# Performance work log

Hardware: AMD Instinct MI355X
Metric: run time of the kernel (lower is better)

Reference implementation:

```python
import jax, jax.numpy as jnp
import numpy as np
from jax import lax

B, C, H, W = 2, 64, 48, 48
NH, DK, DV = 8, 64, 128          # heads, per-head d_k, per-head d_v
DN, NS, R = 128, 16, 4           # SS2D d_inner (expand=2), d_state, dt_rank
MULT = 4                          # FFN expansion
L = H * W


def layer_norm(x, w, b, eps=1e-5):
    m = x.mean(-1, keepdims=True)
    v = ((x - m) ** 2).mean(-1, keepdims=True)
    return (x - m) / jnp.sqrt(v + eps) * w + b


def conv2d(x, w, groups=1):
    # x: NCHW, w: OIHW
    return lax.conv_general_dilated(x, w, (1, 1), 'SAME',
                                    dimension_numbers=('NCHW', 'OIHW', 'NCHW'),
                                    feature_group_count=groups)


def setup_inputs() -> dict:
    key = jax.random.key(0)
    ks = jax.random.split(key, 24)
    rn = lambda k, shp, s=0.02: jax.random.normal(k, shp, jnp.float32) * s
    inp = {
        'enc_input': jax.random.normal(ks[0], (B, C, H, W), jnp.float32),
        'slf_attn_snr': jax.random.uniform(ks[1], (B, 1, H, W), jnp.float32),
        # MultiHeadAttention params
        'attn_wq': rn(ks[2], (C, NH * DK)),
        'attn_wk': rn(ks[3], (C, NH * DK)),
        'attn_wv': rn(ks[4], (C, NH * DV)),
        'attn_fc': rn(ks[5], (NH * DV, C)),
        'attn_ln_w': jnp.ones((C,), jnp.float32),
        'attn_ln_b': jnp.zeros((C,), jnp.float32),
        # SS2D params
        'ss_in_w': rn(ks[6], (C, 2 * DN)),
        'ss_conv_w': rn(ks[7], (DN, 1, 3, 3)),
        'ss_conv_b': jnp.zeros((DN,), jnp.float32),
        'ss_xproj_w': rn(ks[8], (4, R + 2 * NS, DN)),
        'ss_dt_w': rn(ks[9], (4, DN, R)),
        'ss_dt_b': rn(ks[10], (4, DN)),
        'ss_Alog': jnp.log(jnp.broadcast_to(jnp.arange(1, NS + 1, dtype=jnp.float32), (4, DN, NS))),
        'ss_D': jnp.ones((4, DN), jnp.float32),
        'ss_norm_w': jnp.ones((DN,), jnp.float32),
        'ss_norm_b': jnp.zeros((DN,), jnp.float32),
        'ss_out_w': rn(ks[11], (DN, C)),
        # FFN (PreNorm + conv block)
        'ffn_ln_w': jnp.ones((C,), jnp.float32),
        'ffn_ln_b': jnp.zeros((C,), jnp.float32),
        'ffn_w1': rn(ks[12], (C * MULT, C, 1, 1)),
        'ffn_dw': rn(ks[13], (C * MULT, 1, 3, 3)),
        'ffn_w2': rn(ks[14], (C, C * MULT, 1, 1)),
    }
    return inp


def reference(enc_input, slf_attn_snr, attn_wq, attn_wk, attn_wv, attn_fc,
              attn_ln_w, attn_ln_b, ss_in_w, ss_conv_w, ss_conv_b, ss_xproj_w,
              ss_dt_w, ss_dt_b, ss_Alog, ss_D, ss_norm_w, ss_norm_b, ss_out_w,
              ffn_ln_w, ffn_ln_b, ffn_w1, ffn_dw, ffn_w2):
    # ---- Multi-head self-attention over spatial tokens (SNR-biased) ----
    x_tok = enc_input.reshape(B, C, L).transpose(0, 2, 1)        # (B, L, C)
    q = (x_tok @ attn_wq).reshape(B, L, NH, DK).transpose(0, 2, 1, 3)
    k = (x_tok @ attn_wk).reshape(B, L, NH, DK).transpose(0, 2, 1, 3)
    v = (x_tok @ attn_wv).reshape(B, L, NH, DV).transpose(0, 2, 1, 3)
    scores = jnp.einsum('bhqd,bhkd->bhqk', q, k) / jnp.sqrt(jnp.float32(DK))
    snr_flat = slf_attn_snr.reshape(B, 1, 1, L)                  # bias over keys
    scores = scores + jnp.log(snr_flat + 1e-4)
    attn = jax.nn.softmax(scores, axis=-1)                       # (B, NH, L, L)
    o = jnp.einsum('bhqk,bhkd->bhqd', attn, v)
    o = o.transpose(0, 2, 1, 3).reshape(B, L, NH * DV) @ attn_fc
    enc_output = layer_norm(o + x_tok, attn_ln_w, attn_ln_b)     # post-LN residual
    enc_output = enc_output.transpose(0, 2, 1).reshape(B, C, H, W)

    # ---- SS2D: 4-direction 2D selective scan ----
    xh = enc_output.transpose(0, 2, 3, 1)                        # (B, H, W, C)
    snr_h = slf_attn_snr.transpose(0, 2, 3, 1)                   # (B, H, W, 1)
    xz = xh @ ss_in_w                                            # (B, H, W, 2*DN)
    x1, z = xz[..., :DN], xz[..., DN:]
    x1 = x1.transpose(0, 3, 1, 2)                                # (B, DN, H, W)
    x1 = conv2d(x1, ss_conv_w, groups=DN) + ss_conv_b[None, :, None, None]
    x1 = jax.nn.silu(x1)

    x_hw = x1.reshape(B, DN, L)
    x_wh = x1.transpose(0, 1, 3, 2).reshape(B, DN, L)
    xs = jnp.stack([x_hw, x_wh], axis=1)                         # (B, 2, DN, L)
    xs = jnp.concatenate([xs, jnp.flip(xs, axis=-1)], axis=1)    # (B, 4, DN, L)

    x_dbl = jnp.einsum('bkdl,kcd->bkcl', xs, ss_xproj_w)
    dts, Bs, Cs = x_dbl[:, :, :R], x_dbl[:, :, R:R + NS], x_dbl[:, :, R + NS:]
    dts = jnp.einsum('bkrl,kdr->bkdl', dts, ss_dt_w) + ss_dt_b[None, :, :, None]
    dts = jax.nn.softplus(dts)                                   # (B, 4, DN, L)
    A = -jnp.exp(ss_Alog)                                        # (4, DN, NS)

    def step(h, inp):
        xt, dtt, Bt, Ct = inp                                    # (B,4,DN),(B,4,DN),(B,4,NS),(B,4,NS)
        dA = jnp.exp(dtt[..., None] * A)                         # (B,4,DN,NS)
        h = h * dA + (dtt * xt)[..., None] * Bt[:, :, None, :]
        y = jnp.einsum('bkdn,bkn->bkd', h, Ct)
        return h, y

    h0 = jnp.zeros((B, 4, DN, NS), jnp.float32)
    elems = (xs.transpose(3, 0, 1, 2), dts.transpose(3, 0, 1, 2),
             Bs.transpose(3, 0, 1, 2), Cs.transpose(3, 0, 1, 2))
    _, ys = lax.scan(step, h0, elems)                            # (L, B, 4, DN)
    ys = ys.transpose(1, 2, 3, 0) + ss_D[None, :, :, None] * xs  # (B, 4, DN, L)

    inv = jnp.flip(ys[:, 2:4], axis=-1)                          # undo reversed scans
    wh = ys[:, 1].reshape(B, DN, W, H).transpose(0, 1, 3, 2).reshape(B, DN, L)
    invwh = inv[:, 1].reshape(B, DN, W, H).transpose(0, 1, 3, 2).reshape(B, DN, L)
    y = ys[:, 0] + inv[:, 0] + wh + invwh                        # (B, DN, L)
    y = y.transpose(0, 2, 1).reshape(B, H, W, DN)
    y = layer_norm(y, ss_norm_w, ss_norm_b) * jax.nn.silu(z) * snr_h
    x2 = y @ ss_out_w + enc_input.transpose(0, 2, 3, 1)          # (B, H, W, C)

    # ---- PreNorm conv FeedForward ----
    xn = layer_norm(x2, ffn_ln_w, ffn_ln_b).transpose(0, 3, 1, 2)
    h1 = jax.nn.gelu(conv2d(xn, ffn_w1), approximate=False)
    h1 = jax.nn.gelu(conv2d(h1, ffn_dw, groups=C * MULT), approximate=False)
    h1 = conv2d(h1, ffn_w2).transpose(0, 2, 3, 1)
    x3 = h1 + x2

    return x3.transpose(0, 3, 1, 2)                              # (B, C, H, W)
```

## Files before the change

### kernel.cpp

```cpp
#include <hip/hip_runtime.h>
#include <hip/hip_bf16.h>

#define Bq 2
#define Cc 64
#define Hh 48
#define Ww 48
#define Ll 2304
#define NHh 8
#define DKk 64
#define DVv 128
#define DNn 128
#define NSs 16
#define Rr 4
#define SCH 48
#define SNC 48
#define TT 8
#define TT2 16

#define OQ    0u
#define OK_   2359296u
#define OV    4718592u
#define OO    9437184u
#define OX1P  14450688u
#define OZ    15040512u
#define OVT   15630336u
#define OLP   (OVT + 2359296u)
#define OFCB  (OVT + 2433024u)
#define OX2   0u
#define WS_NEED_FLOATS (OVT + 4718592u)
#define ODT2  OQ
#define OYS2  OK_
#define OX1S  (OV + 1179648u)
#define OBS2  (OV + 1769472u)
#define OCS2  (OV + 2064384u)
#define OCSA  (OV + 2359296u)
#define OCSB  (OV + 3145728u)
#define OHST  (OV + 3932160u)
#define OH1A  OO
#define OH1B  (OO + 1179648u)

typedef short short8v __attribute__((ext_vector_type(8)));
typedef short short4v __attribute__((ext_vector_type(4)));
typedef float f32x4 __attribute__((ext_vector_type(4)));
typedef unsigned short ushort_t;

__device__ __forceinline__ float geluf(float x) {
  return 0.5f * x * (1.0f + erff(x * 0.70710678118654752f));
}
__device__ __forceinline__ float siluf(float x) {
  return x / (1.0f + __expf(-x));
}
__device__ __forceinline__ float softplusf(float x) {
  return fmaxf(x, 0.0f) + log1pf(__expf(-fabsf(x)));
}
__device__ __forceinline__ int spmap(int k, int l) {
  if (k == 0) return l;
  if (k == 1) return (l % 48) * 48 + l / 48;
  if (k == 2) return 2303 - l;
  int l2 = 2303 - l; return (l2 % 48) * 48 + l2 / 48;
}
__device__ __forceinline__ short f2bf(float f) {
  unsigned u = __float_as_uint(f);
  unsigned r = (u + 0x7FFFu + ((u >> 16) & 1u)) >> 16;
  return (short)r;
}
__device__ __forceinline__ float bfu2f(ushort_t u) {
  return __uint_as_float(((unsigned)u) << 16);
}

__global__ void k_code(float* out) { if (threadIdx.x == 0) out[0] = 25000.f; }

__global__ __launch_bounds__(256) void k_qkv(const float* __restrict__ enc,
    const float* __restrict__ wq, const float* __restrict__ wk,
    const float* __restrict__ wv, float* __restrict__ ws) {
  int l0 = blockIdx.x * TT; int b = blockIdx.y;
  int t = threadIdx.x;
  __shared__ float xs[64][12];
  {
    int idx = t, c = idx >> 3, i = idx & 7;
    xs[c][i] = enc[(size_t)b * Cc * Ll + (size_t)c * Ll + l0 + i];
    idx = t + 256; c = idx >> 3; i = idx & 7;
    xs[c][i] = enc[(size_t)b * Cc * Ll + (size_t)c * Ll + l0 + i];
  }
  __syncthreads();
  ushort_t* qb = (ushort_t*)(ws + OQ);
  ushort_t* kb = (ushort_t*)(ws + OK_);
  float* v = ws + OV;
#pragma unroll
  for (int g = 0; g < 6; ++g) {
    int j = t + g * 256;
    float acc[TT];
#pragma unroll
    for (int i = 0; i < TT; ++i) acc[i] = 0.f;
    const float* wp; int col, stride;
    if (j < 512) { wp = wq + j; stride = 512; col = j; }
    else if (j < 1024) { wp = wk + (j - 512); stride = 512; col = j - 512; }
    else { wp = wv + (j - 1024); stride = 1024; col = j - 1024; }
    for (int c = 0; c < 64; ++c) {
      float w = wp[(size_t)c * stride];
      const float4* xc = (const float4*)&xs[c][0];
      float4 x0 = xc[0], x1 = xc[1];
      acc[0] += x0.x * w; acc[1] += x0.y * w;
      acc[2] += x0.z * w; acc[3] += x0.w * w;
      acc[4] += x1.x * w; acc[5] += x1.y * w;
      acc[6] += x1.z * w; acc[7] += x1.w * w;
    }
    if (j < 512) {
#pragma unroll
      for (int i = 0; i < TT; ++i)
        qb[((size_t)(b * 8 + (col >> 6)) * Ll + l0 + i) * 64 + (col & 63)] =
            (ushort_t)f2bf(acc[i] * 0.125f);
    } else if (j < 1024) {
#pragma unroll
      for (int i = 0; i < TT; ++i)
        kb[((size_t)(b * 8 + (col >> 6)) * Ll + l0 + i) * 64 + (col & 63)] =
            (ushort_t)f2bf(acc[i]);
    } else {
#pragma unroll
      for (int i = 0; i < TT; ++i)
        v[((size_t)(b * 8 + (col >> 7)) * Ll + l0 + i) * 128 + (col & 127)] = acc[i];
    }
  }
}

__global__ __launch_bounds__(256) void k_vt(float* __restrict__ ws) {
  int bh = blockIdx.y;
  int l0 = blockIdx.x * 64;
  int t = threadIdx.x;
  __shared__ float tile[128][65];
  const float* vp = ws + OV + ((size_t)bh * Ll + l0) * 128;
  for (int i = t; i < 64 * 32; i += 256) {
    int l = i >> 5, dv4 = (i & 31) * 4;
    float4 a = *(const float4*)(vp + (size_t)l * 128 + dv4);
    tile[dv4][l] = a.x; tile[dv4 + 1][l] = a.y;
    tile[dv4 + 2][l] = a.z; tile[dv4 + 3][l] = a.w;
  }
  __syncthreads();
  ushort_t* vt = (ushort_t*)(ws + OVT) + (size_t)bh * 128 * Ll + l0;
  for (int i = t; i < 128 * 16; i += 256) {
    int dv = i >> 4, l4 = (i & 15) * 4;
    short4v a;
    a[0] = f2bf(tile[dv][l4]); a[1] = f2bf(tile[dv][l4 + 1]);
    a[2] = f2bf(tile[dv][l4 + 2]); a[3] = f2bf(tile[dv][l4 + 3]);
    *(short4v*)(vt + (size_t)dv * Ll + l4) = a;
  }
}

__global__ __launch_bounds__(256) void k_fcbf(const float* __restrict__ fc,
                                              float* __restrict__ ws) {
  int col = blockIdx.x;
  int t = threadIdx.x;
  ushort_t* dst = (ushort_t*)(ws + OFCB) + (size_t)col * 1024;
  for (int k = t; k < 1024; k += 256)
    dst[k] = (ushort_t)f2bf(fc[(size_t)k * 64 + col]);
}

#define NKT2 18
#define LSK 72
__global__ __launch_bounds__(256) void k_attn(const float* __restrict__ snr,
                                              float* __restrict__ ws) {
  int bh = blockIdx.y; int b = bh >> 3; int hd = bh & 7;
  int q0 = blockIdx.x * 64;
  int ks = blockIdx.z;
  int kbase = ks * (Ll / 2);
  int t = threadIdx.x;
  int w = t >> 6, lane = t & 63;
  int m16 = lane & 15, quad = lane >> 4;

  __shared__ __align__(16) ushort_t Ks[64 * LSK];
  __shared__ __align__(16) ushort_t Vs[128 * LSK];
  __shared__ __align__(16) ushort_t Ps[4 * 16 * LSK];
  __shared__ float sfac_s[64];

  const ushort_t* qbf = (const ushort_t*)(ws + OQ) + (size_t)bh * Ll * 64;
  const ushort_t* kbf = (const ushort_t*)(ws + OK_) + (size_t)bh * Ll * 64;
  const ushort_t* vtb = (const ushort_t*)(ws + OVT) + (size_t)bh * 128 * Ll;

  short8v qa[2];
  {
    const ushort_t* qrp = qbf + (size_t)(q0 + w * 16 + m16) * 64 + quad * 8;
    qa[0] = *(const short8v*)qrp;
    qa[1] = *(const short8v*)(qrp + 32);
  }
  int sk_key = t >> 2, sk_d0 = (t & 3) * 16;
  int sv_dv = t >> 1, sv_k0 = (t & 1) * 32;

  short8v kreg[2], vreg[4];
  float snr_reg = 0.f;
  {
    const ushort_t* ksrc = kbf + (size_t)(kbase + sk_key) * 64 + sk_d0;
    kreg[0] = *(const short8v*)ksrc;
    kreg[1] = *(const short8v*)(ksrc + 8);
    const ushort_t* vsrc = vtb + (size_t)sv_dv * Ll + kbase + sv_k0;
#pragma unroll
    for (int i = 0; i < 4; ++i) vreg[i] = *(const short8v*)(vsrc + i * 8);
    if (t < 64) snr_reg = snr[b * Ll + kbase + t];
  }

  f32x4 oacc[8];
#pragma unroll
  for (int i = 0; i < 8; ++i) oacc[i] = (f32x4)0.f;
  float l_r[4] = {0.f, 0.f, 0.f, 0.f};

  for (int kt = 0; kt < NKT2; ++kt) {
    __syncthreads();
    *(short8v*)&Ks[sk_key * LSK + sk_d0] = kreg[0];
    *(short8v*)&Ks[sk_key * LSK + sk_d0 + 8] = kreg[1];
#pragma unroll
    for (int i = 0; i < 4; ++i)
      *(short8v*)&Vs[sv_dv * LSK + sv_k0 + i * 8] = vreg[i];
    if (t < 64) sfac_s[t] = snr_reg + 1e-4f;
    __syncthreads();
    if (kt + 1 < NKT2) {
      int k0n = kbase + (kt + 1) * 64;
      const ushort_t* ksrc = kbf + (size_t)(k0n + sk_key) * 64 + sk_d0;
      kreg[0] = *(const short8v*)ksrc;
      kreg[1] = *(const short8v*)(ksrc + 8);
      const ushort_t* vsrc = vtb + (size_t)sv_dv * Ll + k0n + sv_k0;
#pragma unroll
      for (int i = 0; i < 4; ++i) vreg[i] = *(const short8v*)(vsrc + i * 8);
      if (t < 64) snr_reg = snr[b * Ll + k0n + t];
    }

    f32x4 sac[4];
#pragma unroll
    for (int n = 0; n < 4; ++n) {
      int key = n * 16 + m16;
      short8v kb0 = *(const short8v*)&Ks[key * LSK + quad * 8];
      short8v kb1 = *(const short8v*)&Ks[key * LSK + 32 + quad * 8];
      f32x4 acc = (f32x4)0.f;
      acc = __builtin_amdgcn_mfma_f32_16x16x32_bf16(qa[0], kb0, acc, 0, 0, 0);
      acc = __builtin_amdgcn_mfma_f32_16x16x32_bf16(qa[1], kb1, acc, 0, 0, 0);
      sac[n] = acc;
    }
    float sf[4];
#pragma unroll
    for (int n = 0; n < 4; ++n) sf[n] = sfac_s[n * 16 + m16];
    ushort_t* pw = &Ps[w * 16 * LSK];
#pragma unroll
    for (int r = 0; r < 4; ++r) {
#pragma unroll
      for (int n = 0; n < 4; ++n) {
        float p = __expf(sac[n][r]) * sf[n];
        l_r[r] += p;
        pw[(quad * 4 + r) * LSK + n * 16 + m16] = (ushort_t)f2bf(p);
      }
    }
    short8v pb0 = *(const short8v*)&pw[m16 * LSK + quad * 8];
    short8v pb1 = *(const short8v*)&pw[m16 * LSK + 32 + quad * 8];
#pragma unroll
    for (int dt_ = 0; dt_ < 8; ++dt_) {
      const ushort_t* vrow = &Vs[(dt_ * 16 + m16) * LSK];
      short8v va0 = *(const short8v*)&vrow[quad * 8];
      short8v va1 = *(const short8v*)&vrow[32 + quad * 8];
      f32x4 o = oacc[dt_];
      o = __builtin_amdgcn_mfma_f32_16x16x32_bf16(va0, pb0, o, 0, 0, 0);
      o = __builtin_amdgcn_mfma_f32_16x16x32_bf16(va1, pb1, o, 0, 0, 0);
      oacc[dt_] = o;
    }
  }
#pragma unroll
  for (int r = 0; r < 4; ++r) {
    float lv = l_r[r];
    lv += __shfl_xor(lv, 1, 64);
    lv += __shfl_xor(lv, 2, 64);
    lv += __shfl_xor(lv, 4, 64);
    lv += __shfl_xor(lv, 8, 64);
    l_r[r] = lv;
  }
  if (m16 == 0) {
    float* lp = ws + OLP + (size_t)ks * (Bq * NHh * Ll) + (size_t)bh * Ll;
#pragma unroll
    for (int r = 0; r < 4; ++r) lp[q0 + w * 16 + quad * 4 + r] = l_r[r];
  }
  ushort_t* opb = (ushort_t*)(ws + (ks ? OV : OO));
  ushort_t* op = opb + ((size_t)(b * Ll + q0 + w * 16 + m16)) * 1024 + hd * 128;
#pragma unroll
  for (int dt_ = 0; dt_ < 8; ++dt_) {
    short4v o4;
#pragma unroll
    for (int r = 0; r < 4; ++r) o4[r] = f2bf(oacc[dt_][r]);
    *(short4v*)&op[dt_ * 16 + quad * 4] = o4;
  }
}

__global__ __launch_bounds__(256) void k_oprojxz(const float* __restrict__ enc,
    const float* __restrict__ lnw, const float* __restrict__ lnb,
    const float* __restrict__ ssin, float* __restrict__ ws) {
  int l0 = blockIdx.x * TT2, b = blockIdx.y, t = threadIdx.x;
  int w = t >> 6, lane = t & 63, m16 = lane & 15, quad = lane >> 4;
  __shared__ __align__(16) ushort_t obf[16][1040];
  __shared__ float linv_s[8][16];
  __shared__ float part[16][68];
  __shared__ float xh_s[64][17];
  if (t < 128) {
    int hd = t >> 4, i = t & 15;
    float l1 = ws[OLP + (size_t)(b * 8 + hd) * Ll + l0 + i];
    float l2 = ws[OLP + (size_t)(Bq * NHh * Ll) + (size_t)(b * 8 + hd) * Ll + l0 + i];
    linv_s[hd][i] = 1.f / (l1 + l2);
  }
  __syncthreads();
  const ushort_t* p0 = (const ushort_t*)(ws + OO) + (size_t)(b * Ll + l0) * 1024;
  const ushort_t* p1 = (const ushort_t*)(ws + OV) + (size_t)(b * Ll + l0) * 1024;
#pragma unroll
  for (int g = 0; g < 8; ++g) {
    int v = t + g * 256;
    int tok = v >> 7, k0 = (v & 127) * 8;
    short8v a = *(const short8v*)(p0 + (size_t)tok * 1024 + k0);
    short8v bb = *(const short8v*)(p1 + (size_t)tok * 1024 + k0);
    float li = linv_s[k0 >> 7][tok];
    short8v o;
#pragma unroll
    for (int j = 0; j < 8; ++j)
      o[j] = f2bf((bfu2f((ushort_t)a[j]) + bfu2f((ushort_t)bb[j])) * li);
    *(short8v*)&obf[tok][k0] = o;
  }
  __syncthreads();
  f32x4 cacc = (f32x4)0.f;
  const ushort_t* fcb = (const ushort_t*)(ws + OFCB) +
                        (size_t)(w * 16 + m16) * 1024 + quad * 8;
#pragma unroll
  for (int kb = 0; kb < 32; ++kb) {
    short8v a = *(const short8v*)&obf[m16][kb * 32 + quad * 8];
    short8v bf = *(const short8v*)(fcb + kb * 32);
    cacc = __builtin_amdgcn_mfma_f32_16x16x32_bf16(a, bf, cacc, 0, 0, 0);
  }
#pragma unroll
  for (int r = 0; r < 4; ++r) part[quad * 4 + r][w * 16 + m16] = cacc[r];
  __syncthreads();
  {
    int col = lane;
    float lw = lnw[col], lb = lnb[col];
#pragma unroll
    for (int i2 = 0; i2 < 4; ++i2) {
      int i = w * 4 + i2;
      float a = part[i][col] + enc[(size_t)b * Cc * Ll + (size_t)col * Ll + l0 + i];
      float s = a;
#pragma unroll
      for (int o = 32; o >= 1; o >>= 1) s += __shfl_xor(s, o, 64);
      float m = s * (1.f / 64.f);
      float dd = a - m;
      float vs = dd * dd;
#pragma unroll
      for (int o = 32; o >= 1; o >>= 1) vs += __shfl_xor(vs, o, 64);
      xh_s[col][i] = dd * rsqrtf(vs * (1.f / 64.f) + 1e-5f) * lw + lb;
    }
  }
  __syncthreads();
  {
    float acc2[TT2];
#pragma unroll
    for (int i = 0; i < TT2; ++i) acc2[i] = 0.f;
    for (int c = 0; c < 64; ++c) {
      float wv_ = ssin[c * 256 + t];
      const float* xc = &xh_s[c][0];
#pragma unroll
      for (int i = 0; i < TT2; ++i) acc2[i] += xc[i] * wv_;
    }
    if (t < 128) {
#pragma unroll
      for (int i = 0; i < TT2; ++i)
        ws[OX1P + ((size_t)(b * Ll + l0 + i)) * 128 + t] = acc2[i];
    } else {
#pragma unroll
      for (int i = 0; i < TT2; ++i)
        ws[OZ + ((size_t)(b * Ll + l0 + i)) * 128 + (t - 128)] = acc2[i];
    }
  }
}

__global__ __launch_bounds__(256) void k_conv(const float* __restrict__ cw,
    const float* __restrict__ cb, float* __restrict__ ws) {
  int l0 = blockIdx.x * TT, b = blockIdx.y, t = threadIdx.x;
  int h = l0 / 48, w0 = l0 % 48;
  __shared__ float tile[3][10][128];
  for (int idx = t; idx < 3840; idx += 256) {
    int r = idx / 1280, rem = idx % 1280;
    int col = rem >> 7, d = rem & 127;
    int hh = h + r - 1, wx = w0 + col - 1;
    float v = 0.f;
    if (hh >= 0 && hh < 48 && wx >= 0 && wx < 48)
      v = ws[OX1P + ((size_t)(b * Ll + hh * 48 + wx)) * 128 + d];
    tile[r][col][d] = v;
  }
  __syncthreads();
  int d = t & 127, half = t >> 7;
  float cwr[9];
#pragma unroll
  for (int j = 0; j < 9; ++j) cwr[j] = cw[d * 9 + j];
  float cbv = cb[d];
#pragma unroll
  for (int j = 0; j < 4; ++j) {
    int i = half * 4 + j;
    float acc = cbv;
#pragma unroll
    for (int kh = 0; kh < 3; ++kh)
#pragma unroll
      for (int kw = 0; kw < 3; ++kw)
        acc += tile[kh][i + kw][d] * cwr[kh * 3 + kw];
    ws[OX1S + ((size_t)(b * Ll + l0 + i)) * 128 + d] = siluf(acc);
  }
}

__global__ __launch_bounds__(128) void k_xdbl(const float* __restrict__ xw,
    const float* __restrict__ dtw, const float* __restrict__ dtb,
    float* __restrict__ ws) {
  int l0 = blockIdx.x * TT;
  int by = blockIdx.y; int b = by >> 2; int k = by & 3;
  int t = threadIdx.x;
  __shared__ float xv[128][9];
  __shared__ float pr[36][TT];
#pragma unroll
  for (int i = 0; i < TT; ++i) {
    int sp = spmap(k, l0 + i);
    xv[t][i] = ws[OX1S + ((size_t)(b * Ll) + sp) * 128 + t];
  }
  __syncthreads();
  if (t < 36) {
    float s[TT];
#pragma unroll
    for (int i = 0; i < TT; ++i) s[i] = 0.f;
    const float* wp = xw + (size_t)(k * 36 + t) * 128;
    for (int d = 0; d < 128; ++d) {
      float w = wp[d];
      const float* xc = &xv[d][0];
#pragma unroll
      for (int i = 0; i < TT; ++i) s[i] += xc[i] * w;
    }
#pragma unroll
    for (int i = 0; i < TT; ++i) pr[t][i] = s[i];
  }
  __syncthreads();
  {
    int d = t;
    const float* wp = dtw + (size_t)(k * 128 + d) * 4;
    float w0 = wp[0], w1 = wp[1], w2 = wp[2], w3 = wp[3];
    float bb = dtb[k * 128 + d];
#pragma unroll
    for (int i = 0; i < TT; ++i) {
      float v = pr[0][i] * w0 + pr[1][i] * w1 + pr[2][i] * w2 + pr[3][i] * w3 + bb;
      ws[ODT2 + ((size_t)(by * Ll + l0 + i)) * 128 + d] = softplusf(v);
    }
  }
  if (t < 16) {
#pragma unroll
    for (int i = 0; i < TT; ++i)
      ws[OBS2 + ((size_t)(by * Ll + l0 + i)) * 16 + t] = pr[4 + t][i];
  } else if (t < 32) {
#pragma unroll
    for (int i = 0; i < TT; ++i)
      ws[OCS2 + ((size_t)(by * Ll + l0 + i)) * 16 + (t - 16)] = pr[20 + (t - 16)][i];
  }
}

__global__ __launch_bounds__(256) void k_scanA(const float* __restrict__ alog,
                                               float* __restrict__ ws) {
  int c = blockIdx.x;
  int bk = blockIdx.y;
  int b = bk >> 2, k = bk & 3;
  int t = threadIdx.x;
  int n = t & 15, dg = t >> 4;
  __shared__ float dt_s[2][128], x_s[2][128], Bs_s[2][16];
  float A_r[8], ap[8], bc[8];
#pragma unroll
  for (int i = 0; i < 8; ++i) {
    int d = dg * 8 + i;
    A_r[i] = -__expf(alog[(size_t)((k * 128 + d) * 16) + n]);
    ap[i] = 1.f; bc[i] = 0.f;
  }
  const float* dtp = ws + ODT2 + ((size_t)bk * Ll) * 128;
  const float* bsp = ws + OBS2 + ((size_t)bk * Ll) * 16;
  const float* xb = ws + OX1S + (size_t)b * Ll * 128;
  float r_a = 0.f, r_Bs = 0.f;
  {
    int l = c * SCH;
    int sp = spmap(k, l);
    if (t < 128) r_a = dtp[(size_t)l * 128 + t];
    else r_a = xb[(size_t)sp * 128 + (t - 128)];
    if (t < 16) r_Bs = bsp[(size_t)l * 16 + t];
  }
  for (int ll = 0; ll < SCH; ++ll) {
    int buf = ll & 1;
    if (t < 128) dt_s[buf][t] = r_a;
    else x_s[buf][t - 128] = r_a;
    if (t < 16) Bs_s[buf][t] = r_Bs;
    __syncthreads();
    if (ll + 1 < SCH) {
      int l2 = c * SCH + ll + 1;
      int sp2 = spmap(k, l2);
      if (t < 128) r_a = dtp[(size_t)l2 * 128 + t];
      else r_a = xb[(size_t)sp2 * 128 + (t - 128)];
      if (t < 16) r_Bs = bsp[(size_t)l2 * 16 + t];
    }
    float Bv = Bs_s[buf][n];
#pragma unroll
    for (int i = 0; i < 8; ++i) {
      int d = dg * 8 + i;
      float dtv = dt_s[buf][d];
      float a = __expf(dtv * A_r[i]);
      bc[i] = bc[i] * a + dtv * x_s[buf][d] * Bv;
      ap[i] *= a;
    }
  }
  float* csa = ws + OCSA + ((size_t)(bk * SNC + c) * 128) * 16;
  float* csb = ws + OCSB + ((size_t)(bk * SNC + c) * 128) * 16;
#pragma unroll
  for (int i = 0; i < 8; ++i) {
    int d = dg * 8 + i;
    csa[d * 16 + n] = ap[i];
    csb[d * 16 + n] = bc[i];
  }
}

__global__ __launch_bounds__(256) void k_scanB(float* __restrict__ ws) {
  int g = blockIdx.x * 256 + threadIdx.x;
  int bk = g >> 11;
  int dn = g & 2047;
  const float* csa = ws + OCSA;
  const float* csb = ws + OCSB;
  float* hst = ws + OHST;
  size_t base = (size_t)bk * SNC * 2048 + dn;
  float h = 0.f;
  float a = csa[base], bq = csb[base];
  for (int c = 0; c < SNC; ++c) {
    float na = 0.f, nb = 0.f;
    if (c + 1 < SNC) {
      size_t idx2 = base + (size_t)(c + 1) * 2048;
      na = csa[idx2]; nb = csb[idx2];
    }
    hst[base + (size_t)c * 2048] = h;
    h = a * h + bq;
    a = na; bq = nb;
  }
}

__global__ __launch_bounds__(256) void k_scanC(const float* __restrict__ alog,
    const float* __restrict__ Dp, float* __restrict__ ws) {
  int c = blockIdx.x, bk = blockIdx.y;
  int b = bk >> 2, k = bk & 3;
  int t = threadIdx.x;
  int n = t & 15, dg = t >> 4;
  __shared__ float dt_s[2][128], x_s[2][128], Bs_s[2][16], Cs_s[2][16];
  float A_r[8], h[8], Dv[8];
#pragma unroll
  for (int i = 0; i < 8; ++i) {
    int d = dg * 8 + i;
    A_r[i] = -__expf(alog[(size_t)((k * 128 + d) * 16) + n]);
    h[i] = ws[OHST + ((size_t)(bk * SNC + c) * 128 + d) * 16 + n];
    Dv[i] = Dp[k * 128 + d];
  }
  const float* dtp = ws + ODT2 + ((size_t)bk * Ll) * 128;
  const float* bsp = ws + OBS2 + ((size_t)bk * Ll) * 16;
  const float* csp = ws + OCS2 + ((size_t)bk * Ll) * 16;
  const float* xb = ws + OX1S + (size_t)b * Ll * 128;
  float* yp = ws + OYS2 + ((size_t)bk * Ll) * 128;
  float r_a = 0.f, r_bc = 0.f;
  {
    int l = c * SCH;
    int sp = spmap(k, l);
    if (t < 128) r_a = dtp[(size_t)l * 128 + t];
    else r_a = xb[(size_t)sp * 128 + (t - 128)];
    if (t < 16) r_bc = bsp[(size_t)l * 16 + t];
    else if (t < 32) r_bc = csp[(size_t)l * 16 + (t - 16)];
  }
  for (int ll = 0; ll < SCH; ++ll) {
    int buf = ll & 1;
    if (t < 128) dt_s[buf][t] = r_a;
    else x_s[buf][t - 128] = r_a;
    if (t < 16) Bs_s[buf][t] = r_bc;
    else if (t < 32) Cs_s[buf][t - 16] = r_bc;
    __syncthreads();
    if (ll + 1 < SCH) {
      int l2 = c * SCH + ll + 1;
      int sp2 = spmap(k, l2);
      if (t < 128) r_a = dtp[(size_t)l2 * 128 + t];
      else r_a = xb[(size_t)sp2 * 128 + (t - 128)];
      if (t < 16) r_bc = bsp[(size_t)l2 * 16 + t];
      else if (t < 32) r_bc = csp[(size_t)l2 * 16 + (t - 16)];
    }
    int l = c * SCH + ll;
    float Bv = Bs_s[buf][n], Cv = Cs_s[buf][n];
    float yacc[8];
#pragma unroll
    for (int i = 0; i < 8; ++i) {
      int d = dg * 8 + i;
      float dtv = dt_s[buf][d];
      float a = __expf(dtv * A_r[i]);
      h[i] = h[i] * a + dtv * x_s[buf][d] * Bv;
      yacc[i] = h[i] * Cv;
    }
#pragma unroll
    for (int i = 0; i < 8; ++i) {
      float yv = yacc[i];
      yv += __shfl_xor(yv, 1, 64);
      yv += __shfl_xor(yv, 2, 64);
      yv += __shfl_xor(yv, 4, 64);
      yv += __shfl_xor(yv, 8, 64);
      yacc[i] = yv;
    }
    if (n == 0) {
#pragma unroll
      for (int i = 0; i < 8; ++i) {
        int d = dg * 8 + i;
        yp[(size_t)l * 128 + d] = yacc[i] + Dv[i] * x_s[buf][d];
      }
    }
  }
}

__global__ __launch_bounds__(256) void k_combffn1(const float* __restrict__ enc,
    const float* __restrict__ nw, const float* __restrict__ nb,
    const float* __restrict__ snr, const float* __restrict__ ow,
    const float* __restrict__ lw, const float* __restrict__ lb,
    const float* __restrict__ w1, float* __restrict__ ws) {
  int l0 = blockIdx.x * TT, b = blockIdx.y, t = threadIdx.x;
  __shared__ float yr[128][9];
  __shared__ float redm[2][TT], redq[2][TT];
  __shared__ float part[2][TT][64];
  __shared__ float xn_s[64][9];
  int lane = t & 63, wid = (t >> 6) & 1;
  float v[TT], m[TT];
  if (t < 128) {
    int d = t;
    const float* ysb = ws + OYS2;
#pragma unroll
    for (int i = 0; i < TT; ++i) {
      int l = l0 + i;
      int hh = l / 48, wwp = l % 48;
      int lT = wwp * 48 + hh;
      v[i] = ysb[((size_t)(b * 4 + 0) * Ll + l) * 128 + d] +
             ysb[((size_t)(b * 4 + 2) * Ll + (2303 - l)) * 128 + d] +
             ysb[((size_t)(b * 4 + 1) * Ll + lT) * 128 + d] +
             ysb[((size_t)(b * 4 + 3) * Ll + (2303 - lT)) * 128 + d];
    }
    float s[TT];
#pragma unroll
    for (int i = 0; i < TT; ++i) s[i] = v[i];
#pragma unroll
    for (int o = 32; o >= 1; o >>= 1)
#pragma unroll
      for (int i = 0; i < TT; ++i) s[i] += __shfl_xor(s[i], o, 64);
    if (lane == 0) {
#pragma unroll
      for (int i = 0; i < TT; ++i) redm[wid][i] = s[i];
    }
  }
  __syncthreads();
  if (t < 128) {
    float q[TT];
#pragma unroll
    for (int i = 0; i < TT; ++i) {
      m[i] = (redm[0][i] + redm[1][i]) * (1.f / 128.f);
      float dv = v[i] - m[i];
      q[i] = dv * dv;
    }
#pragma unroll
    for (int o = 32; o >= 1; o >>= 1)
#pragma unroll
      for (int i = 0; i < TT; ++i) q[i] += __shfl_xor(q[i], o, 64);
    if (lane == 0) {
#pragma unroll
      for (int i = 0; i < TT; ++i) redq[wid][i] = q[i];
    }
  }
  __syncthreads();
  if (t < 128) {
    int d = t;
    float nwv = nw[d], nbv = nb[d];
#pragma unroll
    for (int i = 0; i < TT; ++i) {
      int l = l0 + i;
      float var = (redq[0][i] + redq[1][i]) * (1.f / 128.f);
      float y = (v[i] - m[i]) * rsqrtf(var + 1e-5f) * nwv + nbv;
      float zv = ws[OZ + ((size_t)(b * Ll + l)) * 128 + d];
      y *= siluf(zv);
      y *= snr[b * Ll + l];
      yr[d][i] = y;
    }
  }
  __syncthreads();
  if (t < 128) {
    int col = t & 63, seg = t >> 6;
    float acc[TT];
#pragma unroll
    for (int i = 0; i < TT; ++i) acc[i] = 0.f;
    const float* ows = ow + (size_t)(seg * 64) * 64 + col;
    for (int c = 0; c < 64; ++c) {
      float w = ows[c * 64];
      const float* yc = &yr[seg * 64 + c][0];
#pragma unroll
      for (int i = 0; i < TT; ++i) acc[i] += yc[i] * w;
    }
#pragma unroll
    for (int i = 0; i < TT; ++i) part[seg][i][col] = acc[i];
  }
  __syncthreads();
  {
    int wv = t >> 6, col2 = t & 63;
    float lwv = lw[col2], lbv = lb[col2];
#pragma unroll
    for (int i2 = 0; i2 < 2; ++i2) {
      int i = wv * 2 + i2;
      float a = part[0][i][col2] + part[1][i][col2];
      a += enc[(size_t)b * Cc * Ll + (size_t)col2 * Ll + l0 + i];
      ws[OX2 + ((size_t)(b * Ll + l0 + i)) * 64 + col2] = a;
      float s = a;
#pragma unroll
      for (int o = 32; o >= 1; o >>= 1) s += __shfl_xor(s, o, 64);
      float mm = s * (1.f / 64.f);
      float dd2 = a - mm;
      float vs = dd2 * dd2;
#pragma unroll
      for (int o = 32; o >= 1; o >>= 1) vs += __shfl_xor(vs, o, 64);
      xn_s[col2][i] = dd2 * rsqrtf(vs * (1.f / 64.f) + 1e-5f) * lwv + lbv;
    }
  }
  __syncthreads();
  {
    float acc2[TT];
#pragma unroll
    for (int i = 0; i < TT; ++i) acc2[i] = 0.f;
    const float* wp = w1 + (size_t)t * 64;
    for (int c = 0; c < 64; ++c) {
      float w = wp[c];
      const float* xc = &xn_s[c][0];
#pragma unroll
      for (int i = 0; i < TT; ++i) acc2[i] += xc[i] * w;
    }
#pragma unroll
    for (int i = 0; i < TT; ++i)
      ws[OH1A + ((size_t)(b * Ll + l0 + i)) * 256 + t] = geluf(acc2[i]);
  }
}

__global__ __launch_bounds__(256) void k_ffndw(const float* __restrict__ dww,
                                               float* __restrict__ ws) {
  int l0 = blockIdx.x * TT, b = blockIdx.y, t = threadIdx.x;
  int h = l0 / 48, w0 = l0 % 48;
  __shared__ float tile[3][10][256];
  for (int idx = t; idx < 7680; idx += 256) {
    int r = idx / 2560, rem = idx % 2560;
    int col = rem >> 8, ch = rem & 255;
    int hh = h + r - 1, wx = w0 + col - 1;
    float v = 0.f;
    if (hh >= 0 && hh < 48 && wx >= 0 && wx < 48)
      v = ws[OH1A + ((size_t)(b * Ll + hh * 48 + wx)) * 256 + ch];
    tile[r][col][ch] = v;
  }
  __syncthreads();
  float dwr[9];
#pragma unroll
  for (int j = 0; j < 9; ++j) dwr[j] = dww[t * 9 + j];
#pragma unroll
  for (int i = 0; i < TT; ++i) {
    float acc = 0.f;
#pragma unroll
    for (int kh = 0; kh < 3; ++kh)
#pragma unroll
      for (int kw = 0; kw < 3; ++kw)
        acc += tile[kh][i + kw][t] * dwr[kh * 3 + kw];
    ws[OH1B + ((size_t)(b * Ll + l0 + i)) * 256 + t] = geluf(acc);
  }
}

__global__ __launch_bounds__(256) void k_ffn2(const float* __restrict__ w2,
                                              float* __restrict__ ws,
                                              float* __restrict__ out) {
  int l0 = blockIdx.x * TT, b = blockIdx.y, t = threadIdx.x;
  __shared__ float hr[256][9];
  __shared__ float part[4][TT][64];
  const float* hp = ws + OH1B + ((size_t)(b * Ll + l0)) * 256;
#pragma unroll
  for (int i = 0; i < TT; ++i) hr[t][i] = hp[(size_t)i * 256 + t];
  __syncthreads();
  int col = t & 63, seg = t >> 6;
  {
    float acc[TT];
#pragma unroll
    for (int i = 0; i < TT; ++i) acc[i] = 0.f;
    const float* wp = w2 + (size_t)col * 256 + seg * 64;
    for (int c = 0; c < 64; ++c) {
      float w = wp[c];
      const float* hc = &hr[seg * 64 + c][0];
#pragma unroll
      for (int i = 0; i < TT; ++i) acc[i] += hc[i] * w;
    }
#pragma unroll
    for (int i = 0; i < TT; ++i) part[seg][i][col] = acc[i];
  }
  __syncthreads();
  if (t < 64) {
    float av[TT];
#pragma unroll
    for (int i = 0; i < TT; ++i) {
      float a = part[0][i][t] + part[1][i][t] + part[2][i][t] + part[3][i][t];
      av[i] = a + ws[OX2 + ((size_t)(b * Ll + l0 + i)) * 64 + t];
    }
    float* opx = out + ((size_t)(b * 64 + t)) * 2304 + l0;
    *(float4*)opx = make_float4(av[0], av[1], av[2], av[3]);
    *((float4*)opx + 1) = make_float4(av[4], av[5], av[6], av[7]);
  }
}

extern "C" void kernel_launch(void* const* d_in, const int* in_sizes, int n_in,
                              void* d_out, int out_size, void* d_ws, size_t ws_size,
                              hipStream_t stream) {
  (void)in_sizes; (void)n_in; (void)out_size;
  const float* enc  = (const float*)d_in[0];
  const float* snr  = (const float*)d_in[1];
  const float* wq   = (const float*)d_in[2];
  const float* wk   = (const float*)d_in[3];
  const float* wv   = (const float*)d_in[4];
  const float* fc   = (const float*)d_in[5];
  const float* alnw = (const float*)d_in[6];
  const float* alnb = (const float*)d_in[7];
  const float* ssin = (const float*)d_in[8];
  const float* cw   = (const float*)d_in[9];
  const float* cb   = (const float*)d_in[10];
  const float* xw   = (const float*)d_in[11];
  const float* dtw  = (const float*)d_in[12];
  const float* dtb  = (const float*)d_in[13];
  const float* alog = (const float*)d_in[14];
  const float* Dp   = (const float*)d_in[15];
  const float* nw   = (const float*)d_in[16];
  const float* nb   = (const float*)d_in[17];
  const float* ow   = (const float*)d_in[18];
  const float* flnw = (const float*)d_in[19];
  const float* flnb = (const float*)d_in[20];
  const float* w1   = (const float*)d_in[21];
  const float* dww  = (const float*)d_in[22];
  const float* w2   = (const float*)d_in[23];
  float* ws = (float*)d_ws;
  float* out = (float*)d_out;

  if (ws_size < (size_t)WS_NEED_FLOATS * 4) {
    hipLaunchKernelGGL(k_code, dim3(1), dim3(64), 0, stream, out);
    return;
  }

  hipLaunchKernelGGL(k_qkv, dim3(Ll / TT, Bq), dim3(256), 0, stream, enc, wq, wk, wv, ws);
  hipLaunchKernelGGL(k_vt, dim3(Ll / 64, Bq * NHh), dim3(256), 0, stream, ws);
  hipLaunchKernelGGL(k_fcbf, dim3(64), dim3(256), 0, stream, fc, ws);
  hipLaunchKernelGGL(k_attn, dim3(Ll / 64, Bq * NHh, 2), dim3(256), 0, stream, snr, ws);
  hipLaunchKernelGGL(k_oprojxz, dim3(Ll / TT2, Bq), dim3(256), 0, stream, enc, alnw, alnb, ssin, ws);
  hipLaunchKernelGGL(k_conv, dim3(Ll / TT, Bq), dim3(256), 0, stream, cw, cb, ws);
  hipLaunchKernelGGL(k_xdbl, dim3(Ll / TT, Bq * 4), dim3(128), 0, stream, xw, dtw, dtb, ws);
  hipLaunchKernelGGL(k_scanA, dim3(SNC, Bq * 4), dim3(256), 0, stream, alog, ws);
  hipLaunchKernelGGL(k_scanB, dim3(64), dim3(256), 0, stream, ws);
  hipLaunchKernelGGL(k_scanC, dim3(SNC, Bq * 4), dim3(256), 0, stream, alog, Dp, ws);
  hipLaunchKernelGGL(k_combffn1, dim3(Ll / TT, Bq), dim3(256), 0, stream, enc, nw, nb, snr, ow, flnw, flnb, w1, ws);
  hipLaunchKernelGGL(k_ffndw, dim3(Ll / TT, Bq), dim3(256), 0, stream, dww, ws);
  hipLaunchKernelGGL(k_ffn2, dim3(Ll / TT, Bq), dim3(256), 0, stream, w2, ws, out);
}
```

Baseline: 415.0 us.

## Use bf16 MFMA for QKV projection and fuse depthwise conv with FFN2

A new prep kernel converts the Q/K/V weights to transposed bf16. The QKV projection is then rewritten to use 16x16x32 bf16 MFMA over 16-token tiles, replacing the scalar fp32 FMA loop. The fc bf16 conversion is folded into extra blocks of the V-transpose kernel, and the depthwise conv is fused with the second FFN pointwise conv so the intermediate never goes through global memory. The cost is lower precision on the QKV inputs (bf16 activations and weights), plus an extra small prep launch each call.

Result: faster. 395.8 us (-4.6%).

```diff
diff --git a/kernel.cpp b/kernel.cpp
--- a/kernel.cpp
+++ b/kernel.cpp
@@ -26,6 +26,7 @@
 #define OVT   15630336u
 #define OLP   (OVT + 2359296u)
 #define OFCB  (OVT + 2433024u)
+#define OWQKV (OFCB + 32768u)
 #define OX2   0u
 #define WS_NEED_FLOATS (OVT + 4718592u)
 #define ODT2  OQ
@@ -37,7 +38,6 @@
 #define OCSB  (OV + 3145728u)
 #define OHST  (OV + 3932160u)
 #define OH1A  OO
-#define OH1B  (OO + 1179648u)
 
 typedef short short8v __attribute__((ext_vector_type(8)));
 typedef short short4v __attribute__((ext_vector_type(4)));
@@ -70,63 +70,102 @@
 
 __global__ void k_code(float* out) { if (threadIdx.x == 0) out[0] = 25000.f; }
 
+__global__ __launch_bounds__(256) void k_prep(const float* __restrict__ wq,
+    const float* __restrict__ wk, const float* __restrict__ wv,
+    float* __restrict__ ws) {
+  int col0 = blockIdx.x * 16;
+  int t = threadIdx.x;
+  ushort_t* dst = (ushort_t*)(ws + OWQKV);
+#pragma unroll
+  for (int g = 0; g < 4; ++g) {
+    int e = t + g * 256;
+    int c = e >> 4, lcol = e & 15;
+    int col = col0 + lcol;
+    float v;
+    if (col < 512) v = wq[(size_t)c * 512 + col];
+    else if (col < 1024) v = wk[(size_t)c * 512 + (col - 512)];
+    else v = wv[(size_t)c * 1024 + (col - 1024)];
+    dst[(size_t)col * 64 + c] = (ushort_t)f2bf(v);
+  }
+}
+
 __global__ __launch_bounds__(256) void k_qkv(const float* __restrict__ enc,
-    const float* __restrict__ wq, const float* __restrict__ wk,
-    const float* __restrict__ wv, float* __restrict__ ws) {
-  int l0 = blockIdx.x * TT; int b = blockIdx.y;
+                                             float* __restrict__ ws) {
+  int l0 = blockIdx.x * TT2; int b = blockIdx.y; int z = blockIdx.z;
   int t = threadIdx.x;
-  __shared__ float xs[64][12];
-  {
-    int idx = t, c = idx >> 3, i = idx & 7;
-    xs[c][i] = enc[(size_t)b * Cc * Ll + (size_t)c * Ll + l0 + i];
-    idx = t + 256; c = idx >> 3; i = idx & 7;
-    xs[c][i] = enc[(size_t)b * Cc * Ll + (size_t)c * Ll + l0 + i];
-  }
-  __syncthreads();
+  int w = t >> 6, lane = t & 63, m16 = lane & 15, quad = lane >> 4;
+  __shared__ __align__(16) ushort_t xs[16][72];
+  {
+    int e = t * 4;
+    int c = e >> 4, tok0 = e & 15;
+    float4 a = *(const float4*)(enc + (size_t)b * Cc * Ll + (size_t)c * Ll + l0 + tok0);
+    xs[tok0][c] = (ushort_t)f2bf(a.x);
+    xs[tok0 + 1][c] = (ushort_t)f2bf(a.y);
+    xs[tok0 + 2][c] = (ushort_t)f2bf(a.z);
+    xs[tok0 + 3][c] = (ushort_t)f2bf(a.w);
+  }
+  __syncthreads();
+  short8v qa0 = *(const short8v*)&xs[m16][quad * 8];
+  short8v qa1 = *(const short8v*)&xs[m16][32 + quad * 8];
   ushort_t* qb = (ushort_t*)(ws + OQ);
   ushort_t* kb = (ushort_t*)(ws + OK_);
   float* v = ws + OV;
-#pragma unroll
-  for (int g = 0; g < 6; ++g) {
-    int j = t + g * 256;
-    float acc[TT];
-#pragma unroll
-    for (int i = 0; i < TT; ++i) acc[i] = 0.f;
-    const float* wp; int col, stride;
-    if (j < 512) { wp = wq + j; stride = 512; col = j; }
-    else if (j < 1024) { wp = wk + (j - 512); stride = 512; col = j - 512; }
-    else { wp = wv + (j - 1024); stride = 1024; col = j - 1024; }
-    for (int c = 0; c < 64; ++c) {
-      float w = wp[(size_t)c * stride];
-      const float4* xc = (const float4*)&xs[c][0];
-      float4 x0 = xc[0], x1 = xc[1];
-      acc[0] += x0.x * w; acc[1] += x0.y * w;
-      acc[2] += x0.z * w; acc[3] += x0.w * w;
-      acc[4] += x1.x * w; acc[5] += x1.y * w;
-      acc[6] += x1.z * w; acc[7] += x1.w * w;
-    }
-    if (j < 512) {
-#pragma unroll
-      for (int i = 0; i < TT; ++i)
-        qb[((size_t)(b * 8 + (col >> 6)) * Ll + l0 + i) * 64 + (col & 63)] =
-            (ushort_t)f2bf(acc[i] * 0.125f);
-    } else if (j < 1024) {
-#pragma unroll
-      for (int i = 0; i < TT; ++i)
-        kb[((size_t)(b * 8 + (col >> 6)) * Ll + l0 + i) * 64 + (col & 63)] =
-            (ushort_t)f2bf(acc[i]);
+  const ushort_t* wb = (const ushort_t*)(ws + OWQKV);
+#pragma unroll
+  for (int it = 0; it < 8; ++it) {
+    int j0 = z * 512 + it * 64 + w * 16;
+    const ushort_t* bp = wb + (size_t)(j0 + m16) * 64 + quad * 8;
+    short8v b0 = *(const short8v*)bp;
+    short8v b1 = *(const short8v*)(bp + 32);
+    f32x4 cacc = (f32x4)0.f;
+    cacc = __builtin_amdgcn_mfma_f32_16x16x32_bf16(qa0, b0, cacc, 0, 0, 0);
+    cacc = __builtin_amdgcn_mfma_f32_16x16x32_bf16(qa1, b1, cacc, 0, 0, 0);
+    int col = j0 + m16;
+    if (col < 512) {
+#pragma unroll
+      for (int r = 0; r < 4; ++r) {
+        int tok = quad * 4 + r;
+        qb[((size_t)(b * 8 + (col >> 6)) * Ll + l0 + tok) * 64 + (col & 63)] =
+            (ushort_t)f2bf(cacc[r] * 0.125f);
+      }
+    } else if (col < 1024) {
+      int cc = col - 512;
+#pragma unroll
+      for (int r = 0; r < 4; ++r) {
+        int tok = quad * 4 + r;
+        kb[((size_t)(b * 8 + (cc >> 6)) * Ll + l0 + tok) * 64 + (cc & 63)] =
+            (ushort_t)f2bf(cacc[r]);
+      }
     } else {
-#pragma unroll
-      for (int i = 0; i < TT; ++i)
-        v[((size_t)(b * 8 + (col >> 7)) * Ll + l0 + i) * 128 + (col & 127)] = acc[i];
-    }
-  }
-}
-
-__global__ __launch_bounds__(256) void k_vt(float* __restrict__ ws) {
+      int cc = col - 1024;
+#pragma unroll
+      for (int r = 0; r < 4; ++r) {
+        int tok = quad * 4 + r;
+        v[((size_t)(b * 8 + (cc >> 7)) * Ll + l0 + tok) * 128 + (cc & 127)] = cacc[r];
+      }
+    }
+  }
+}
+
+__global__ __launch_bounds__(256) void k_vt(const float* __restrict__ fc,
+                                            float* __restrict__ ws) {
+  int t = threadIdx.x;
+  if (blockIdx.y == 16) {
+    int col0 = blockIdx.x * 2;
+    if (col0 < 64) {
+      ushort_t* dst = (ushort_t*)(ws + OFCB);
+#pragma unroll
+      for (int g = 0; g < 8; ++g) {
+        int e = t + g * 256;
+        int lc = e >> 10, k = e & 1023;
+        dst[(size_t)(col0 + lc) * 1024 + k] =
+            (ushort_t)f2bf(fc[(size_t)k * 64 + col0 + lc]);
+      }
+    }
+    return;
+  }
   int bh = blockIdx.y;
   int l0 = blockIdx.x * 64;
-  int t = threadIdx.x;
   __shared__ float tile[128][65];
   const float* vp = ws + OV + ((size_t)bh * Ll + l0) * 128;
   for (int i = t; i < 64 * 32; i += 256) {
@@ -144,15 +183,6 @@
     a[2] = f2bf(tile[dv][l4 + 2]); a[3] = f2bf(tile[dv][l4 + 3]);
     *(short4v*)(vt + (size_t)dv * Ll + l4) = a;
   }
-}
-
-__global__ __launch_bounds__(256) void k_fcbf(const float* __restrict__ fc,
-                                              float* __restrict__ ws) {
-  int col = blockIdx.x;
-  int t = threadIdx.x;
-  ushort_t* dst = (ushort_t*)(ws + OFCB) + (size_t)col * 1024;
-  for (int k = t; k < 1024; k += 256)
-    dst[k] = (ushort_t)f2bf(fc[(size_t)k * 64 + col]);
 }
 
 #define NKT2 18
@@ -733,11 +763,14 @@
   }
 }
 
-__global__ __launch_bounds__(256) void k_ffndw(const float* __restrict__ dww,
-                                               float* __restrict__ ws) {
+__global__ __launch_bounds__(256) void k_ffndw2(const float* __restrict__ dww,
+    const float* __restrict__ w2, float* __restrict__ ws,
+    float* __restrict__ out) {
   int l0 = blockIdx.x * TT, b = blockIdx.y, t = threadIdx.x;
   int h = l0 / 48, w0 = l0 % 48;
-  __shared__ float tile[3][10][256];
+  __shared__ float smem[3 * 10 * 256];
+  __shared__ float part[4][TT][64];
+  float* tile = smem;
   for (int idx = t; idx < 7680; idx += 256) {
     int r = idx / 2560, rem = idx % 2560;
     int col = rem >> 8, ch = rem & 255;
@@ -745,12 +778,13 @@
     float v = 0.f;
     if (hh >= 0 && hh < 48 && wx >= 0 && wx < 48)
       v = ws[OH1A + ((size_t)(b * Ll + hh * 48 + wx)) * 256 + ch];
-    tile[r][col][ch] = v;
+    tile[r * 2560 + col * 256 + ch] = v;
   }
   __syncthreads();
   float dwr[9];
 #pragma unroll
   for (int j = 0; j < 9; ++j) dwr[j] = dww[t * 9 + j];
+  float hv[TT];
 #pragma unroll
   for (int i = 0; i < TT; ++i) {
     float acc = 0.f;
@@ -758,20 +792,13 @@
     for (int kh = 0; kh < 3; ++kh)
 #pragma unroll
       for (int kw = 0; kw < 3; ++kw)
-        acc += tile[kh][i + kw][t] * dwr[kh * 3 + kw];
-    ws[OH1B + ((size_t)(b * Ll + l0 + i)) * 256 + t] = geluf(acc);
-  }
-}
-
-__global__ __launch_bounds__(256) void k_ffn2(const float* __restrict__ w2,
-                                              float* __restrict__ ws,
-                                              float* __restrict__ out) {
-  int l0 = blockIdx.x * TT, b = blockIdx.y, t = threadIdx.x;
-  __shared__ float hr[256][9];
-  __shared__ float part[4][TT][64];
-  const float* hp = ws + OH1B + ((size_t)(b * Ll + l0)) * 256;
-#pragma unroll
-  for (int i = 0; i < TT; ++i) hr[t][i] = hp[(size_t)i * 256 + t];
+        acc += tile[kh * 2560 + (i + kw) * 256 + t] * dwr[kh * 3 + kw];
+    hv[i] = geluf(acc);
+  }
+  __syncthreads();
+  float* hr = smem;
+#pragma unroll
+  for (int i = 0; i < TT; ++i) hr[t * 9 + i] = hv[i];
   __syncthreads();
   int col = t & 63, seg = t >> 6;
   {
@@ -781,7 +808,7 @@
     const float* wp = w2 + (size_t)col * 256 + seg * 64;
     for (int c = 0; c < 64; ++c) {
       float w = wp[c];
-      const float* hc = &hr[seg * 64 + c][0];
+      const float* hc = &hr[(seg * 64 + c) * 9];
 #pragma unroll
       for (int i = 0; i < TT; ++i) acc[i] += hc[i] * w;
     }
@@ -838,9 +865,9 @@
     return;
   }
 
-  hipLaunchKernelGGL(k_qkv, dim3(Ll / TT, Bq), dim3(256), 0, stream, enc, wq, wk, wv, ws);
-  hipLaunchKernelGGL(k_vt, dim3(Ll / 64, Bq * NHh), dim3(256), 0, stream, ws);
-  hipLaunchKernelGGL(k_fcbf, dim3(64), dim3(256), 0, stream, fc, ws);
+  hipLaunchKernelGGL(k_prep, dim3(128), dim3(256), 0, stream, wq, wk, wv, ws);
+  hipLaunchKernelGGL(k_qkv, dim3(Ll / TT2, Bq, 4), dim3(256), 0, stream, enc, ws);
+  hipLaunchKernelGGL(k_vt, dim3(Ll / 64, 17), dim3(256), 0, stream, fc, ws);
   hipLaunchKernelGGL(k_attn, dim3(Ll / 64, Bq * NHh, 2), dim3(256), 0, stream, snr, ws);
   hipLaunchKernelGGL(k_oprojxz, dim3(Ll / TT2, Bq), dim3(256), 0, stream, enc, alnw, alnb, ssin, ws);
   hipLaunchKernelGGL(k_conv, dim3(Ll / TT, Bq), dim3(256), 0, stream, cw, cb, ws);
@@ -849,6 +876,5 @@
   hipLaunchKernelGGL(k_scanB, dim3(64), dim3(256), 0, stream, ws);
   hipLaunchKernelGGL(k_scanC, dim3(SNC, Bq * 4), dim3(256), 0, stream, alog, Dp, ws);
   hipLaunchKernelGGL(k_combffn1, dim3(Ll / TT, Bq), dim3(256), 0, stream, enc, nw, nb, snr, ow, flnw, flnb, w1, ws);
-  hipLaunchKernelGGL(k_ffndw, dim3(Ll / TT, Bq), dim3(256), 0, stream, dww, ws);
-  hipLaunchKernelGGL(k_ffn2, dim3(Ll / TT, Bq), dim3(256), 0, stream, w2, ws, out);
-}
+  hipLaunchKernelGGL(k_ffndw2, dim3(Ll / TT, Bq), dim3(256), 0, stream, dww, w2, ws, out);
+}
```
